# Performance work log

Measured on AMD Instinct MI355X. Metric: run time of the kernel, lower is better.

The kernel has to match this reference:

```python
import jax, jax.numpy as jnp
import numpy as np

# Static model dims
B, N, EMB, D, H, HD, L, NC = 1, 4096, 1024, 512, 8, 64, 2, 2
# Per-head local neighborhood sizes (round(pi*local_k^2) in the original, static here)
K_PER_HEAD = (32, 48, 64, 80, 96, 112, 128, 160)
SCALE = float(np.sqrt(HD))  # sigma_sq = sqrt(head_dim) in the original


def _ln(x, g, b, eps=1e-5):
    m = x.mean(-1, keepdims=True)
    v = ((x - m) ** 2).mean(-1, keepdims=True)
    return (x - m) * jax.lax.rsqrt(v + eps) * g + b


def _gather(a, idx):
    # a: [B, N, ...], idx: [B, N, K] -> [B, N, K, ...] (per-batch row gather, as k_h[range(B), indices])
    return jax.vmap(lambda ah, ih: ah[ih])(a, idx)


def setup_inputs() -> dict:
    key = jax.random.key(0)
    ks = iter(jax.random.split(key, 48))
    w = lambda shape: 0.02 * jax.random.normal(next(ks), shape, jnp.float32)
    return {
        "x": jax.random.normal(next(ks), (B, N, EMB), jnp.float32),
        "distance": 10.0 * jax.random.uniform(next(ks), (B, N, N), jnp.float32),
        "indices": jax.random.randint(next(ks), (B, N, K_PER_HEAD[-1]), 0, N, jnp.int32),
        "row": jax.random.randint(next(ks), (B, N), 0, 128, jnp.int32),
        "col": jax.random.randint(next(ks), (B, N), 0, 128, jnp.int32),
        # adapter (ResidualFullyConnected, simplified: linear proj + 1 residual layer)
        "adapter_w": w((EMB, D)), "adapter_b": jnp.zeros((D,), jnp.float32),
        "res_w": w((D, D)), "res_b": jnp.zeros((D,), jnp.float32),
        # per-block params, stacked over depth L
        "ln1_g": jnp.ones((L, D), jnp.float32), "ln1_b": jnp.zeros((L, D), jnp.float32),
        "qkv_w": w((L, D, 3 * D)), "qkv_b": jnp.zeros((L, 3 * D), jnp.float32),
        "proj_w": w((L, D, D)), "proj_b": jnp.zeros((L, D), jnp.float32),
        "ln2_g": jnp.ones((L, D), jnp.float32), "ln2_b": jnp.zeros((L, D), jnp.float32),
        "fc1_w": w((L, D, 4 * D)), "fc1_b": jnp.zeros((L, 4 * D), jnp.float32),
        "fc2_w": w((L, 4 * D, D)), "fc2_b": jnp.zeros((L, D), jnp.float32),
        # per-head decay rate parameter (DecayNetwork lambda_p); reparam = softplus
        "lam": 0.5 + w((L, H)),
        "lnf_g": jnp.ones((D,), jnp.float32), "lnf_b": jnp.zeros((D,), jnp.float32),
        "head_w": w((D, NC)), "head_b": jnp.zeros((NC,), jnp.float32),
    }


def _forward(x, distance, indices, adapter_w, adapter_b, res_w, res_b,
             ln1_g, ln1_b, qkv_w, qkv_b, proj_w, proj_b,
             ln2_g, ln2_b, fc1_w, fc1_b, fc2_w, fc2_b,
             lam, lnf_g, lnf_b, head_w, head_b):
    h = x @ adapter_w + adapter_b
    h = h + jax.nn.relu(h @ res_w + res_b)  # residual adapter layer
    for l in range(L):
        # --- spatial multi-head attention with per-head KNN window + decay log-bias ---
        xa = _ln(h, ln1_g[l], ln1_b[l])
        qkv = (xa @ qkv_w[l] + qkv_b[l]).reshape(B, N, 3, H, HD).transpose(2, 0, 3, 1, 4)
        q, k, v = qkv[0], qkv[1], qkv[2]          # [B,H,N,d]
        qn = jnp.sum(q * q, -1)                    # [B,H,N]  |q|^2
        kn = jnp.sum(k * k, -1)                    # [B,H,N]  |k|^2
        heads = []
        for hh in range(H):
            Kh = K_PER_HEAD[hh]
            idx = indices[:, :, :Kh]               # [B,N,Kh] nearest neighbors
            ksel = _gather(k[:, hh], idx)          # [B,N,Kh,d]
            vsel = _gather(v[:, hh], idx)          # [B,N,Kh,d]
            knsel = _gather(kn[:, hh], idx)        # [B,N,Kh]
            attn = jnp.einsum('bnd,bnkd->bnk', q[:, hh], ksel) / SCALE
            attn = attn - 0.5 * (qn[:, hh][..., None] + knsel) / SCALE  # norm correction
            dsel = jnp.take_along_axis(distance, idx, axis=-1)          # [B,N,Kh]
            decay = jnp.exp(-jax.nn.softplus(lam[l, hh]) * dsel) + 1e-6
            attn = jax.nn.softmax(attn + jnp.log(decay), axis=-1)
            heads.append(jnp.einsum('bnk,bnkd->bnd', attn, vsel))
        xo = jnp.stack(heads, 2).reshape(B, N, D)  # [B,N,H,d] -> [B,N,D]
        h = h + (xo @ proj_w[l] + proj_b[l])
        # --- MLP ---
        xm = _ln(h, ln2_g[l], ln2_b[l])
        h = h + (jax.nn.gelu(xm @ fc1_w[l] + fc1_b[l]) @ fc2_w[l] + fc2_b[l])
    h = _ln(h, lnf_g, lnf_b, eps=1e-6)
    return h.mean(axis=1) @ head_w + head_b  # avg pool + head -> [B, num_classes]


def reference(x, distance, indices, row, col, adapter_w, adapter_b, res_w, res_b,
              ln1_g, ln1_b, qkv_w, qkv_b, proj_w, proj_b,
              ln2_g, ln2_b, fc1_w, fc1_b, fc2_w, fc2_b,
              lam, lnf_g, lnf_b, head_w, head_b):
    # row/col are carried as metadata in the original forward and unused by the math
    return _forward(x, distance, indices, adapter_w, adapter_b, res_w, res_b,
                    ln1_g, ln1_b, qkv_w, qkv_b, proj_w, proj_b,
                    ln2_g, ln2_b, fc1_w, fc1_b, fc2_w, fc2_b,
                    lam, lnf_g, lnf_b, head_w, head_b)
```

## Files before the change

kernel.cpp:

```cpp
#include <hip/hip_runtime.h>
#include <hip/hip_bf16.h>

#define NTOK 4096
#define EMB 1024
#define DMODEL 512
#define NHEAD 8
#define NLAYER 2
#define NCLS 2
#define KMAX 160

typedef __attribute__((ext_vector_type(8))) short bf16x8;
typedef __attribute__((ext_vector_type(4))) float f32x4;

__device__ inline unsigned short f2b(float f) {
    unsigned u = __float_as_uint(f);
    u = u + 0x7FFFu + ((u >> 16) & 1u);
    return (unsigned short)(u >> 16);
}
__device__ inline float b2f(unsigned short s) {
    return __uint_as_float((unsigned)s << 16);
}

__device__ inline float dot2bf(unsigned a, unsigned b, float c) {
    float d;
    asm("v_dot2_f32_bf16 %0, %1, %2, %3" : "=v"(d) : "v"(a), "v"(b), "v"(c));
    return d;
}

__device__ inline float wsum(float v) {
    for (int o = 32; o > 0; o >>= 1) v += __shfl_xor(v, o, 64);
    return v;
}
__device__ inline float wmax(float v) {
    for (int o = 32; o > 0; o >>= 1) v = fmaxf(v, __shfl_xor(v, o, 64));
    return v;
}

typedef __attribute__((address_space(3))) unsigned lds_u32_t;
typedef __attribute__((address_space(1))) const unsigned glb_u32_t;
__device__ inline void gload16(const void* g, void* l) {
    __builtin_amdgcn_global_load_lds((glb_u32_t*)(unsigned long long)g,
                                     (lds_u32_t*)(unsigned)(unsigned long long)l,
                                     16, 0, 0);
}

__device__ const int g_s0cnt[8]  = {682, 342, 622, 822, 954, 993, 899, 607};
__device__ const int g_s0h[8]    = {7, 7, 6, 5, 4, 3, 2, 1};
__device__ const int g_s0base[8] = {0, 682, 402, 202, 70, 31, 125, 417};
__device__ const int g_s1cnt[8]  = {0, 402, 202, 70, 31, 125, 417, 1024};
__device__ const int g_s1h[8]    = {0, 6, 5, 4, 3, 2, 1, 0};
#define ATTN_BLOCKS (1631 * 8)

struct WSeg { const float* src; unsigned short* dst; int K; int N; int tile0; };
struct Prep { WSeg s[6]; const float* x; unsigned short* xb; int xtile0; };

__global__ __launch_bounds__(256) void prep_k(Prep p)
{
    __shared__ unsigned short tile[64][72];
    int t0 = blockIdx.x;
    if (t0 >= p.xtile0) {
        int i = ((t0 - p.xtile0) * 256 + threadIdx.x) * 8;
        float4 a = *(const float4*)(p.x + i);
        float4 b = *(const float4*)(p.x + i + 4);
        unsigned short o[8];
        o[0] = f2b(a.x); o[1] = f2b(a.y); o[2] = f2b(a.z); o[3] = f2b(a.w);
        o[4] = f2b(b.x); o[5] = f2b(b.y); o[6] = f2b(b.z); o[7] = f2b(b.w);
        *(uint4*)(p.xb + i) = *(const uint4*)o;
        return;
    }
    int si = 0;
#pragma unroll
    for (int i = 1; i < 6; i++) if (t0 >= p.s[i].tile0) si = i;
    const float* src0 = p.s[si].src;
    unsigned short* dst0 = p.s[si].dst;
    int K = p.s[si].K, N = p.s[si].N;
    int lt = t0 - p.s[si].tile0;
    int tx = K >> 6, ty = N >> 6;
    int per = tx * ty;
    int l = lt / per, rr = lt - l * per;
    int k0 = (rr % tx) << 6, n0 = (rr / tx) << 6;
    size_t ls = (size_t)K * N * l;
    const float* Wl = src0 + ls;
    unsigned short* Wtl = dst0 + ls;

    int t = threadIdx.x;
    int kl = t >> 2, nb = (t & 3) * 16;
    const float* src = Wl + (size_t)(k0 + kl) * N + n0 + nb;
#pragma unroll
    for (int i = 0; i < 4; i++) {
        float4 v = *(const float4*)(src + 4 * i);
        tile[nb + 4 * i + 0][kl] = f2b(v.x);
        tile[nb + 4 * i + 1][kl] = f2b(v.y);
        tile[nb + 4 * i + 2][kl] = f2b(v.z);
        tile[nb + 4 * i + 3][kl] = f2b(v.w);
    }
    __syncthreads();
    int nl = t >> 2, ks = (t & 3) * 16;
    unsigned short* dst = Wtl + (size_t)(n0 + nl) * K + k0 + ks;
    *(uint4*)dst = *(const uint4*)&tile[nl][ks];
    *(uint4*)(dst + 8) = *(const uint4*)&tile[nl][ks + 8];
}

__global__ __launch_bounds__(256) void dsel_k(const float* __restrict__ distance,
                                              const int* __restrict__ indices,
                                              float* __restrict__ dsel)
{
    int n = blockIdx.x, t = threadIdx.x;
    if (t < KMAX) {
        int idx = indices[(size_t)n * KMAX + t];
        dsel[(size_t)n * KMAX + t] = distance[(size_t)n * NTOK + idx];
    }
}

template <int BM, int BN, int WM, int WN, int MODE>
__global__ __launch_bounds__(256) void mgemm_k(
    const unsigned short* __restrict__ A, const unsigned short* __restrict__ Wt,
    const float* __restrict__ bias, const float* __restrict__ resid,
    float* __restrict__ Cf, unsigned short* __restrict__ Cb,
    float* __restrict__ knout,
    int M, int N, int K)
{
    constexpr int SM = BM / WM;
    constexpr int SN = BN / WN;
    constexpr int MR = SM / 16;
    constexpr int NR = SN / 16;

    __shared__ unsigned short Asl[2][BM * 64];
    __shared__ unsigned short Bsl[2][BN * 64];

    int tid = threadIdx.x;
    int bm = blockIdx.x * BM, bn = blockIdx.y * BN;
    int lane = tid & 63, wid = tid >> 6;
    int wm = wid / WN, wn = wid % WN;
    int l15 = lane & 15, l4 = lane >> 4;

    f32x4 acc[MR][NR] = {};

    auto stage = [&](int buf, int k0) {
#pragma unroll
        for (int i = 0; i < BM / 32; i++) {
            int ci = i * 256 + tid;
            int r = ci >> 3, c = ci & 7;
            gload16(A + (size_t)(bm + r) * K + k0 + ((c ^ (r & 7)) * 8),
                    &Asl[buf][ci * 8]);
        }
#pragma unroll
        for (int i = 0; i < BN / 32; i++) {
            int ci = i * 256 + tid;
            int r = ci >> 3, c = ci & 7;
            gload16(Wt + (size_t)(bn + r) * K + k0 + ((c ^ (r & 7)) * 8),
                    &Bsl[buf][ci * 8]);
        }
    };

    int nt = K / 64;
    stage(0, 0);
    __syncthreads();
    int cur = 0;
    for (int t = 0; t < nt; t++) {
        if (t + 1 < nt) stage(cur ^ 1, (t + 1) * 64);
#pragma unroll
        for (int ks = 0; ks < 2; ks++) {
            bf16x8 af[MR], bfr[NR];
#pragma unroll
            for (int mr = 0; mr < MR; mr++) {
                int ar = wm * SM + mr * 16 + l15;
                af[mr] = *(const bf16x8*)&Asl[cur][ar * 64 + ((((ks << 2) | l4) ^ (ar & 7)) * 8)];
            }
#pragma unroll
            for (int nr = 0; nr < NR; nr++) {
                int br = wn * SN + nr * 16 + l15;
                bfr[nr] = *(const bf16x8*)&Bsl[cur][br * 64 + ((((ks << 2) | l4) ^ (br & 7)) * 8)];
            }
#pragma unroll
            for (int mr = 0; mr < MR; mr++)
#pragma unroll
                for (int nr = 0; nr < NR; nr++)
                    acc[mr][nr] = __builtin_amdgcn_mfma_f32_16x16x32_bf16(af[mr], bfr[nr], acc[mr][nr], 0, 0, 0);
        }
        __syncthreads();
        cur ^= 1;
    }

#pragma unroll
    for (int mr = 0; mr < MR; mr++) {
#pragma unroll
        for (int nr = 0; nr < NR; nr++) {
            int col = bn + wn * SN + nr * 16 + l15;
            float bcol = bias[col];
#pragma unroll
            for (int r = 0; r < 4; r++) {
                int row = bm + wm * SM + mr * 16 + l4 * 4 + r;
                size_t off = (size_t)row * N + col;
                float v = acc[mr][nr][r] + bcol;
                if (MODE == 0) {
                    Cf[off] = v;
                } else if (MODE == 1) {
                    Cf[off] = resid[off] + fmaxf(v, 0.f);
                } else if (MODE == 2) {
                    float t3 = tanhf(0.7978845608028654f * (v + 0.044715f * v * v * v));
                    Cb[off] = f2b(0.5f * v * (1.f + t3));
                } else if (MODE == 3) {
                    Cf[off] = resid[off] + v;
                } else if (MODE == 4) {
                    Cf[off] = v;
                    Cb[off] = f2b(v);
                } else {
                    Cb[off] = f2b(v);
                }
            }
        }
    }

    if (MODE == 5) {
        int cbase = bn + wn * SN;
        if (cbase >= 512 && cbase < 1024) {
            int hh = (cbase - 512) >> 6;
#pragma unroll
            for (int mr = 0; mr < MR; mr++) {
#pragma unroll
                for (int r = 0; r < 4; r++) {
                    float p = 0.f;
#pragma unroll
                    for (int nr = 0; nr < NR; nr++) {
                        float v = acc[mr][nr][r] + bias[cbase + nr * 16 + l15];
                        p += v * v;
                    }
                    p += __shfl_xor(p, 1, 64);
                    p += __shfl_xor(p, 2, 64);
                    p += __shfl_xor(p, 4, 64);
                    p += __shfl_xor(p, 8, 64);
                    if (l15 == 0) {
                        int row = bm + wm * SM + mr * 16 + l4 * 4 + r;
                        knout[row * NHEAD + hh] = p;
                    }
                }
            }
        }
    }
}

template <int OUTB>
__global__ __launch_bounds__(256) void ln_k(
    const float* __restrict__ X, const float* __restrict__ g,
    const float* __restrict__ bta, void* __restrict__ Yv, float eps)
{
    int row = blockIdx.x;
    int tid = threadIdx.x;
    const float* xr = X + (size_t)row * DMODEL;
    float v0 = xr[tid], v1 = xr[tid + 256];
    __shared__ float red[8];
    float s = wsum(v0 + v1);
    int wid = tid >> 6, lane = tid & 63;
    if (lane == 0) red[wid] = s;
    __syncthreads();
    float m = (red[0] + red[1] + red[2] + red[3]) * (1.f / DMODEL);
    float d0 = v0 - m, d1 = v1 - m;
    float sq = wsum(d0 * d0 + d1 * d1);
    if (lane == 0) red[4 + wid] = sq;
    __syncthreads();
    float var = (red[4] + red[5] + red[6] + red[7]) * (1.f / DMODEL);
    float rs = 1.0f / sqrtf(var + eps);
    float y0 = d0 * rs * g[tid] + bta[tid];
    float y1 = d1 * rs * g[tid + 256] + bta[tid + 256];
    if (OUTB) {
        unsigned short* Y = (unsigned short*)Yv;
        Y[(size_t)row * DMODEL + tid] = f2b(y0);
        Y[(size_t)row * DMODEL + tid + 256] = f2b(y1);
    } else {
        float* Y = (float*)Yv;
        Y[(size_t)row * DMODEL + tid] = y0;
        Y[(size_t)row * DMODEL + tid + 256] = y1;
    }
}

__global__ __launch_bounds__(256) void attn_k(
    const unsigned short* __restrict__ qkv,
    const float* __restrict__ kn,
    const int* __restrict__ indices, const float* __restrict__ dsel,
    const float* __restrict__ lam, unsigned short* __restrict__ xo, int layer)
{
    int xcd = blockIdx.x & 7;
    int t = blockIdx.x >> 3;
    int hh, blk;
    int c0 = g_s0cnt[xcd];
    if (t < c0) {
        hh = g_s0h[xcd]; blk = g_s0base[xcd] + t;
    } else {
        t -= c0;
        if (t < g_s1cnt[xcd]) {
            hh = g_s1h[xcd]; blk = t;
        } else {
            return;
        }
    }

    int wid = threadIdx.x >> 6, lane = threadIdx.x & 63;
    int n = blk * 4 + wid;
    int Kh = 32 + 16 * hh + (hh == 7 ? 16 : 0);

    __shared__ __align__(16) unsigned qsp[4][32];
    __shared__ float asc[4][KMAX];
    __shared__ int   sidx[4][KMAX];

    const unsigned short* qrow = qkv + (size_t)n * 1536 + hh * 64;
    float qd = b2f(qrow[lane]);
    if (lane < 32) qsp[wid][lane] = ((const unsigned*)qrow)[lane];
    float qn2 = wsum(qd * qd);
    float sp = log1pf(expf(lam[layer * NHEAD + hh]));

    const int* irow = indices + (size_t)n * KMAX;
    const float* drow = dsel + (size_t)n * KMAX;

    int sub = lane & 3, grp = lane >> 2;
    const uint4* qp = (const uint4*)&qsp[wid][0];
    uint4 qa = qp[sub], qb = qp[4 + sub];

    int iters = Kh >> 4;
    int idxn = irow[grp];
    const uint4* krn = (const uint4*)(qkv + (size_t)idxn * 1536 + 512 + hh * 64);
    uint4 kan = krn[sub], kbn = krn[4 + sub];
    for (int it = 0; it < iters; it++) {
        int idxc = idxn;
        uint4 ka = kan, kb = kbn;
        if (it + 1 < iters) {
            idxn = irow[(it + 1) * 16 + grp];
            const uint4* kr = (const uint4*)(qkv + (size_t)idxn * 1536 + 512 + hh * 64);
            kan = kr[sub]; kbn = kr[4 + sub];
        }
        float d0 = 0.f, d1 = 0.f, d2 = 0.f, d3 = 0.f;
        d0 = dot2bf(ka.x, qa.x, d0); d1 = dot2bf(ka.y, qa.y, d1);
        d2 = dot2bf(ka.z, qa.z, d2); d3 = dot2bf(ka.w, qa.w, d3);
        d0 = dot2bf(kb.x, qb.x, d0); d1 = dot2bf(kb.y, qb.y, d1);
        d2 = dot2bf(kb.z, qb.z, d2); d3 = dot2bf(kb.w, qb.w, d3);
        float dp = (d0 + d1) + (d2 + d3);
        dp += __shfl_xor(dp, 1, 64);
        dp += __shfl_xor(dp, 2, 64);
        if (sub == 0) {
            int kk = it * 16 + grp;
            asc[wid][kk] = dp;
            sidx[wid][kk] = idxc;
        }
    }

    float s0 = -1e30f, s1 = -1e30f, s2 = -1e30f;
    {
        int kk = lane;
        if (kk < Kh) {
            float knv = kn[sidx[wid][kk] * NHEAD + hh];
            s0 = (asc[wid][kk] - 0.5f * (qn2 + knv)) * 0.125f - sp * drow[kk];
        }
        kk = lane + 64;
        if (kk < Kh) {
            float knv = kn[sidx[wid][kk] * NHEAD + hh];
            s1 = (asc[wid][kk] - 0.5f * (qn2 + knv)) * 0.125f - sp * drow[kk];
        }
        kk = lane + 128;
        if (kk < Kh) {
            float knv = kn[sidx[wid][kk] * NHEAD + hh];
            s2 = (asc[wid][kk] - 0.5f * (qn2 + knv)) * 0.125f - sp * drow[kk];
        }
    }
    float mx = wmax(fmaxf(fmaxf(s0, s1), s2));
    float e0 = (s0 > -1e29f) ? expf(s0 - mx) : 0.f;
    float e1 = (s1 > -1e29f) ? expf(s1 - mx) : 0.f;
    float e2 = (s2 > -1e29f) ? expf(s2 - mx) : 0.f;
    float se = wsum(e0 + e1 + e2);
    float inv = 1.f / se;
    if (lane < Kh)       asc[wid][lane]       = e0 * inv;
    if (lane + 64 < Kh)  asc[wid][lane + 64]  = e1 * inv;
    if (lane + 128 < Kh) asc[wid][lane + 128] = e2 * inv;

    int g = lane >> 3, q = lane & 7;
    const uint4* vb = (const uint4*)(qkv + 1024 + hh * 64 + q * 8);
    float a8[8] = {};
    int k0 = 0;
    int kmain = Kh & ~31;
    for (; k0 < kmain; k0 += 32) {
        int ii[4]; float aa[4]; uint4 vv[4];
#pragma unroll
        for (int u = 0; u < 4; u++) {
            int kk = k0 + u * 8 + g;
            ii[u] = sidx[wid][kk];
            aa[u] = asc[wid][kk];
        }
#pragma unroll
        for (int u = 0; u < 4; u++) vv[u] = vb[(size_t)ii[u] * 192];
#pragma unroll
        for (int u = 0; u < 4; u++) {
            const unsigned short* vp = (const unsigned short*)&vv[u];
#pragma unroll
            for (int d = 0; d < 8; d++) a8[d] += aa[u] * b2f(vp[d]);
        }
    }
    if (Kh & 16) {
        int ii[2]; float aa[2]; uint4 vv[2];
#pragma unroll
        for (int u = 0; u < 2; u++) {
            int kk = k0 + u * 8 + g;
            ii[u] = sidx[wid][kk];
            aa[u] = asc[wid][kk];
        }
#pragma unroll
        for (int u = 0; u < 2; u++) vv[u] = vb[(size_t)ii[u] * 192];
#pragma unroll
        for (int u = 0; u < 2; u++) {
            const unsigned short* vp = (const unsigned short*)&vv[u];
#pragma unroll
            for (int d = 0; d < 8; d++) a8[d] += aa[u] * b2f(vp[d]);
        }
    }
#pragma unroll
    for (int d = 0; d < 8; d++) {
        a8[d] += __shfl_xor(a8[d], 8, 64);
        a8[d] += __shfl_xor(a8[d], 16, 64);
        a8[d] += __shfl_xor(a8[d], 32, 64);
    }
    if (lane < 8) {
        unsigned o[4];
#pragma unroll
        for (int p = 0; p < 4; p++)
            o[p] = ((unsigned)f2b(a8[2 * p + 1]) << 16) | (unsigned)f2b(a8[2 * p]);
        *(uint4*)(xo + (size_t)n * DMODEL + hh * 64 + lane * 8) = *(uint4*)o;
    }
}

__global__ __launch_bounds__(512) void colpart_k(const float* __restrict__ Y, float* __restrict__ part)
{
    int c = threadIdx.x;
    int blk = blockIdx.x;
    const float* p = Y + (size_t)blk * 16 * DMODEL + c;
    float s = 0.f;
#pragma unroll
    for (int r = 0; r < 16; r++) s += p[r * DMODEL];
    part[blk * DMODEL + c] = s;
}

__global__ __launch_bounds__(512) void finhead_k(
    const float* __restrict__ part, const float* __restrict__ head_w,
    const float* __restrict__ head_b, float* __restrict__ out)
{
    __shared__ float mv[DMODEL];
    int c = threadIdx.x;
    float s = 0.f;
    for (int i = 0; i < 256; i++) s += part[i * DMODEL + c];
    mv[c] = s * (1.f / NTOK);
    __syncthreads();
    if (c < 64) {
        float a0 = 0.f, a1 = 0.f;
        for (int d = c; d < DMODEL; d += 64) {
            float m = mv[d];
            a0 += m * head_w[d * NCLS + 0];
            a1 += m * head_w[d * NCLS + 1];
        }
        a0 = wsum(a0);
        a1 = wsum(a1);
        if (c == 0) { out[0] = a0 + head_b[0]; out[1] = a1 + head_b[1]; }
    }
}

extern "C" void kernel_launch(void* const* d_in, const int* in_sizes, int n_in,
                              void* d_out, int out_size, void* d_ws, size_t ws_size,
                              hipStream_t stream)
{
    const float* x        = (const float*)d_in[0];
    const float* distance = (const float*)d_in[1];
    const int*   indices  = (const int*)d_in[2];
    const float* adapter_w = (const float*)d_in[5];
    const float* adapter_b = (const float*)d_in[6];
    const float* res_w     = (const float*)d_in[7];
    const float* res_b     = (const float*)d_in[8];
    const float* ln1_g     = (const float*)d_in[9];
    const float* ln1_b     = (const float*)d_in[10];
    const float* qkv_w     = (const float*)d_in[11];
    const float* qkv_b     = (const float*)d_in[12];
    const float* proj_w    = (const float*)d_in[13];
    const float* proj_b    = (const float*)d_in[14];
    const float* ln2_g     = (const float*)d_in[15];
    const float* ln2_b     = (const float*)d_in[16];
    const float* fc1_w     = (const float*)d_in[17];
    const float* fc1_b     = (const float*)d_in[18];
    const float* fc2_w     = (const float*)d_in[19];
    const float* fc2_b     = (const float*)d_in[20];
    const float* lam       = (const float*)d_in[21];
    const float* lnf_g     = (const float*)d_in[22];
    const float* lnf_b     = (const float*)d_in[23];
    const float* head_w    = (const float*)d_in[24];
    const float* head_b    = (const float*)d_in[25];
    float* out = (float*)d_out;

    char* wsb = (char*)d_ws;
    float* h   = (float*)(wsb);
    float* h0  = (float*)(wsb + (8u << 20));
    float* dsel = (float*)(wsb + (8u << 20));
    char* shared = wsb + (16u << 20);
    unsigned short* xb    = (unsigned short*)shared;
    unsigned short* qkvbb = (unsigned short*)shared;
    unsigned short* fc1b  = (unsigned short*)shared;
    unsigned short* adapter_wt = (unsigned short*)(shared + (8u << 20));
    unsigned short* res_wt     = (unsigned short*)(shared + (9u << 20));
    unsigned short* lnb  = (unsigned short*)(wsb + (40u << 20));
    unsigned short* h0b  = lnb;
    unsigned short* xob  = (unsigned short*)(wsb + (44u << 20));
    unsigned short* qkv_wt = (unsigned short*)(wsb + (48u << 20));
    unsigned short* proj_wt = (unsigned short*)(wsb + (51u << 20));
    unsigned short* fc1_wt  = (unsigned short*)(wsb + (52u << 20));
    unsigned short* fc2_wt  = (unsigned short*)(wsb + (56u << 20));
    float* kn   = (float*)(wsb + (60u << 20));
    float* part = (float*)(wsb + (60u << 20) + (1u << 18));

    dim3 blk(256);

    {
        Prep p;
        p.s[0] = { adapter_w, adapter_wt, EMB,    DMODEL, 0 };
        p.s[1] = { res_w,     res_wt,     DMODEL, DMODEL, 128 };
        p.s[2] = { qkv_w,     qkv_wt,     DMODEL, 1536,   192 };
        p.s[3] = { proj_w,    proj_wt,    DMODEL, DMODEL, 576 };
        p.s[4] = { fc1_w,     fc1_wt,     DMODEL, 2048,   704 };
        p.s[5] = { fc2_w,     fc2_wt,     2048,   DMODEL, 1216 };
        p.x = x; p.xb = xb; p.xtile0 = 1728;
        prep_k<<<1728 + (NTOK * EMB) / 2048, blk, 0, stream>>>(p);
    }

    mgemm_k<64, 64, 2, 2, 4><<<dim3(NTOK / 64, DMODEL / 64), blk, 0, stream>>>(
        xb, adapter_wt, adapter_b, nullptr, h0, h0b, nullptr, NTOK, DMODEL, EMB);
    mgemm_k<64, 64, 2, 2, 1><<<dim3(NTOK / 64, DMODEL / 64), blk, 0, stream>>>(
        h0b, res_wt, res_b, h0, h, nullptr, nullptr, NTOK, DMODEL, DMODEL);

    dsel_k<<<NTOK, blk, 0, stream>>>(distance, indices, dsel);

    for (int l = 0; l < NLAYER; l++) {
        ln_k<1><<<NTOK, blk, 0, stream>>>(h, ln1_g + l * DMODEL, ln1_b + l * DMODEL, lnb, 1e-5f);
        mgemm_k<64, 128, 2, 2, 5><<<dim3(NTOK / 64, 1536 / 128), blk, 0, stream>>>(
            lnb, qkv_wt + (size_t)l * 1536 * DMODEL, qkv_b + l * 1536, nullptr,
            nullptr, qkvbb, kn, NTOK, 1536, DMODEL);
        attn_k<<<ATTN_BLOCKS, blk, 0, stream>>>(qkvbb, kn, indices, dsel, lam, xob, l);
        mgemm_k<64, 64, 2, 2, 3><<<dim3(NTOK / 64, DMODEL / 64), blk, 0, stream>>>(
            xob, proj_wt + (size_t)l * DMODEL * DMODEL, proj_b + l * DMODEL, h,
            h, nullptr, nullptr, NTOK, DMODEL, DMODEL);
        ln_k<1><<<NTOK, blk, 0, stream>>>(h, ln2_g + l * DMODEL, ln2_b + l * DMODEL, lnb, 1e-5f);
        mgemm_k<64, 128, 2, 2, 2><<<dim3(NTOK / 64, 2048 / 128), blk, 0, stream>>>(
            lnb, fc1_wt + (size_t)l * 2048 * DMODEL, fc1_b + l * 2048, nullptr,
            nullptr, fc1b, nullptr, NTOK, 2048, DMODEL);
        mgemm_k<64, 64, 2, 2, 3><<<dim3(NTOK / 64, DMODEL / 64), blk, 0, stream>>>(
            fc1b, fc2_wt + (size_t)l * DMODEL * 2048, fc2_b + l * DMODEL, h,
            h, nullptr, nullptr, NTOK, DMODEL, 2048);
    }

    ln_k<0><<<NTOK, blk, 0, stream>>>(h, lnf_g, lnf_b, h0, 1e-6f);
    colpart_k<<<256, 512, 0, stream>>>(h0, part);
    finhead_k<<<1, 512, 0, stream>>>(part, head_w, head_b, out);
}
```

Baseline: 315.9 us.

## Fuse dsel gather into prep, fuse final LN with pooling, single-buffer GEMM

Moves the distance gather into the prep kernel and fuses the final layernorm with the column-sum pooling, removing two launches and an intermediate buffer. The GEMM drops LDS double buffering in favour of a load-sync-compute loop. This cuts LDS use and may raise occupancy, but it also stops loads from overlapping with MFMA work. Attention drops the per-row query-norm term, which cancels under softmax. It computes log(exp(-sp*d)+1e-6) explicitly instead of -sp*d, and applies the softmax normalisation after the V reduction.

```diff
diff --git a/kernel.cpp b/kernel.cpp
--- a/kernel.cpp
+++ b/kernel.cpp
@@ -52,12 +52,24 @@
 #define ATTN_BLOCKS (1631 * 8)
 
 struct WSeg { const float* src; unsigned short* dst; int K; int N; int tile0; };
-struct Prep { WSeg s[6]; const float* x; unsigned short* xb; int xtile0; };
+struct Prep {
+    WSeg s[6];
+    const float* x; unsigned short* xb; int xtile0;
+    const float* distance; const int* indices; float* dsel; int dtile0;
+};
 
 __global__ __launch_bounds__(256) void prep_k(Prep p)
 {
     __shared__ unsigned short tile[64][72];
     int t0 = blockIdx.x;
+    if (t0 >= p.dtile0) {
+        int n = t0 - p.dtile0, t = threadIdx.x;
+        if (t < KMAX) {
+            int idx = p.indices[(size_t)n * KMAX + t];
+            p.dsel[(size_t)n * KMAX + t] = p.distance[(size_t)n * NTOK + idx];
+        }
+        return;
+    }
     if (t0 >= p.xtile0) {
         int i = ((t0 - p.xtile0) * 256 + threadIdx.x) * 8;
         float4 a = *(const float4*)(p.x + i);
@@ -101,17 +113,6 @@
     *(uint4*)(dst + 8) = *(const uint4*)&tile[nl][ks + 8];
 }
 
-__global__ __launch_bounds__(256) void dsel_k(const float* __restrict__ distance,
-                                              const int* __restrict__ indices,
-                                              float* __restrict__ dsel)
-{
-    int n = blockIdx.x, t = threadIdx.x;
-    if (t < KMAX) {
-        int idx = indices[(size_t)n * KMAX + t];
-        dsel[(size_t)n * KMAX + t] = distance[(size_t)n * NTOK + idx];
-    }
-}
-
 template <int BM, int BN, int WM, int WN, int MODE>
 __global__ __launch_bounds__(256) void mgemm_k(
     const unsigned short* __restrict__ A, const unsigned short* __restrict__ Wt,
@@ -125,8 +126,8 @@
     constexpr int MR = SM / 16;
     constexpr int NR = SN / 16;
 
-    __shared__ unsigned short Asl[2][BM * 64];
-    __shared__ unsigned short Bsl[2][BN * 64];
+    __shared__ unsigned short Asl[BM * 64];
+    __shared__ unsigned short Bsl[BN * 64];
 
     int tid = threadIdx.x;
     int bm = blockIdx.x * BM, bn = blockIdx.y * BN;
@@ -136,41 +137,39 @@
 
     f32x4 acc[MR][NR] = {};
 
-    auto stage = [&](int buf, int k0) {
+    auto stage = [&](int k0) {
 #pragma unroll
         for (int i = 0; i < BM / 32; i++) {
             int ci = i * 256 + tid;
             int r = ci >> 3, c = ci & 7;
             gload16(A + (size_t)(bm + r) * K + k0 + ((c ^ (r & 7)) * 8),
-                    &Asl[buf][ci * 8]);
+                    &Asl[ci * 8]);
         }
 #pragma unroll
         for (int i = 0; i < BN / 32; i++) {
             int ci = i * 256 + tid;
             int r = ci >> 3, c = ci & 7;
             gload16(Wt + (size_t)(bn + r) * K + k0 + ((c ^ (r & 7)) * 8),
-                    &Bsl[buf][ci * 8]);
+                    &Bsl[ci * 8]);
         }
     };
 
     int nt = K / 64;
-    stage(0, 0);
-    __syncthreads();
-    int cur = 0;
     for (int t = 0; t < nt; t++) {
-        if (t + 1 < nt) stage(cur ^ 1, (t + 1) * 64);
+        stage(t * 64);
+        __syncthreads();
 #pragma unroll
         for (int ks = 0; ks < 2; ks++) {
             bf16x8 af[MR], bfr[NR];
 #pragma unroll
             for (int mr = 0; mr < MR; mr++) {
                 int ar = wm * SM + mr * 16 + l15;
-                af[mr] = *(const bf16x8*)&Asl[cur][ar * 64 + ((((ks << 2) | l4) ^ (ar & 7)) * 8)];
+                af[mr] = *(const bf16x8*)&Asl[ar * 64 + ((((ks << 2) | l4) ^ (ar & 7)) * 8)];
             }
 #pragma unroll
             for (int nr = 0; nr < NR; nr++) {
                 int br = wn * SN + nr * 16 + l15;
-                bfr[nr] = *(const bf16x8*)&Bsl[cur][br * 64 + ((((ks << 2) | l4) ^ (br & 7)) * 8)];
+                bfr[nr] = *(const bf16x8*)&Bsl[br * 64 + ((((ks << 2) | l4) ^ (br & 7)) * 8)];
             }
 #pragma unroll
             for (int mr = 0; mr < MR; mr++)
@@ -179,7 +178,6 @@
                     acc[mr][nr] = __builtin_amdgcn_mfma_f32_16x16x32_bf16(af[mr], bfr[nr], acc[mr][nr], 0, 0, 0);
         }
         __syncthreads();
-        cur ^= 1;
     }
 
 #pragma unroll
@@ -240,10 +238,9 @@
     }
 }
 
-template <int OUTB>
 __global__ __launch_bounds__(256) void ln_k(
     const float* __restrict__ X, const float* __restrict__ g,
-    const float* __restrict__ bta, void* __restrict__ Yv, float eps)
+    const float* __restrict__ bta, unsigned short* __restrict__ Y, float eps)
 {
     int row = blockIdx.x;
     int tid = threadIdx.x;
@@ -261,17 +258,36 @@
     __syncthreads();
     float var = (red[4] + red[5] + red[6] + red[7]) * (1.f / DMODEL);
     float rs = 1.0f / sqrtf(var + eps);
-    float y0 = d0 * rs * g[tid] + bta[tid];
-    float y1 = d1 * rs * g[tid + 256] + bta[tid + 256];
-    if (OUTB) {
-        unsigned short* Y = (unsigned short*)Yv;
-        Y[(size_t)row * DMODEL + tid] = f2b(y0);
-        Y[(size_t)row * DMODEL + tid + 256] = f2b(y1);
-    } else {
-        float* Y = (float*)Yv;
-        Y[(size_t)row * DMODEL + tid] = y0;
-        Y[(size_t)row * DMODEL + tid + 256] = y1;
-    }
+    Y[(size_t)row * DMODEL + tid] = f2b(d0 * rs * g[tid] + bta[tid]);
+    Y[(size_t)row * DMODEL + tid + 256] = f2b(d1 * rs * g[tid + 256] + bta[tid + 256]);
+}
+
+__global__ __launch_bounds__(512) void lnfcol_k(
+    const float* __restrict__ X, const float* __restrict__ g,
+    const float* __restrict__ bta, float* __restrict__ part)
+{
+    int c = threadIdx.x;
+    int blk = blockIdx.x;
+    __shared__ float redA[8], redB[8];
+    int wid = c >> 6, lane = c & 63;
+    float gc = g[c], bc = bta[c];
+    float acc = 0.f;
+    for (int r = 0; r < 16; r++) {
+        float v = X[(size_t)(blk * 16 + r) * DMODEL + c];
+        float s = wsum(v);
+        if (lane == 0) redA[wid] = s;
+        __syncthreads();
+        float m = (redA[0] + redA[1] + redA[2] + redA[3] +
+                   redA[4] + redA[5] + redA[6] + redA[7]) * (1.f / DMODEL);
+        float d = v - m;
+        float sq = wsum(d * d);
+        if (lane == 0) redB[wid] = sq;
+        __syncthreads();
+        float var = (redB[0] + redB[1] + redB[2] + redB[3] +
+                     redB[4] + redB[5] + redB[6] + redB[7]) * (1.f / DMODEL);
+        acc += d * (1.0f / sqrtf(var + 1e-6f)) * gc + bc;
+    }
+    part[(size_t)blk * DMODEL + c] = acc;
 }
 
 __global__ __launch_bounds__(256) void attn_k(
@@ -304,9 +320,7 @@
     __shared__ int   sidx[4][KMAX];
 
     const unsigned short* qrow = qkv + (size_t)n * 1536 + hh * 64;
-    float qd = b2f(qrow[lane]);
     if (lane < 32) qsp[wid][lane] = ((const unsigned*)qrow)[lane];
-    float qn2 = wsum(qd * qd);
     float sp = log1pf(expf(lam[layer * NHEAD + hh]));
 
     const int* irow = indices + (size_t)n * KMAX;
@@ -348,17 +362,20 @@
         int kk = lane;
         if (kk < Kh) {
             float knv = kn[sidx[wid][kk] * NHEAD + hh];
-            s0 = (asc[wid][kk] - 0.5f * (qn2 + knv)) * 0.125f - sp * drow[kk];
+            float dec = expf(-sp * drow[kk]) + 1e-6f;
+            s0 = (asc[wid][kk] - 0.5f * knv) * 0.125f + logf(dec);
         }
         kk = lane + 64;
         if (kk < Kh) {
             float knv = kn[sidx[wid][kk] * NHEAD + hh];
-            s1 = (asc[wid][kk] - 0.5f * (qn2 + knv)) * 0.125f - sp * drow[kk];
+            float dec = expf(-sp * drow[kk]) + 1e-6f;
+            s1 = (asc[wid][kk] - 0.5f * knv) * 0.125f + logf(dec);
         }
         kk = lane + 128;
         if (kk < Kh) {
             float knv = kn[sidx[wid][kk] * NHEAD + hh];
-            s2 = (asc[wid][kk] - 0.5f * (qn2 + knv)) * 0.125f - sp * drow[kk];
+            float dec = expf(-sp * drow[kk]) + 1e-6f;
+            s2 = (asc[wid][kk] - 0.5f * knv) * 0.125f + logf(dec);
         }
     }
     float mx = wmax(fmaxf(fmaxf(s0, s1), s2));
@@ -367,9 +384,9 @@
     float e2 = (s2 > -1e29f) ? expf(s2 - mx) : 0.f;
     float se = wsum(e0 + e1 + e2);
     float inv = 1.f / se;
-    if (lane < Kh)       asc[wid][lane]       = e0 * inv;
-    if (lane + 64 < Kh)  asc[wid][lane + 64]  = e1 * inv;
-    if (lane + 128 < Kh) asc[wid][lane + 128] = e2 * inv;
+    if (lane < Kh)       asc[wid][lane]       = e0;
+    if (lane + 64 < Kh)  asc[wid][lane + 64]  = e1;
+    if (lane + 128 < Kh) asc[wid][lane + 128] = e2;
 
     int g = lane >> 3, q = lane & 7;
     const uint4* vb = (const uint4*)(qkv + 1024 + hh * 64 + q * 8);
@@ -415,6 +432,7 @@
         a8[d] += __shfl_xor(a8[d], 8, 64);
         a8[d] += __shfl_xor(a8[d], 16, 64);
         a8[d] += __shfl_xor(a8[d], 32, 64);
+        a8[d] *= inv;
     }
     if (lane < 8) {
         unsigned o[4];
@@ -423,17 +441,6 @@
             o[p] = ((unsigned)f2b(a8[2 * p + 1]) << 16) | (unsigned)f2b(a8[2 * p]);
         *(uint4*)(xo + (size_t)n * DMODEL + hh * 64 + lane * 8) = *(uint4*)o;
     }
-}
-
-__global__ __launch_bounds__(512) void colpart_k(const float* __restrict__ Y, float* __restrict__ part)
-{
-    int c = threadIdx.x;
-    int blk = blockIdx.x;
-    const float* p = Y + (size_t)blk * 16 * DMODEL + c;
-    float s = 0.f;
-#pragma unroll
-    for (int r = 0; r < 16; r++) s += p[r * DMODEL];
-    part[blk * DMODEL + c] = s;
 }
 
 __global__ __launch_bounds__(512) void finhead_k(
@@ -492,13 +499,13 @@
     char* wsb = (char*)d_ws;
     float* h   = (float*)(wsb);
     float* h0  = (float*)(wsb + (8u << 20));
-    float* dsel = (float*)(wsb + (8u << 20));
     char* shared = wsb + (16u << 20);
     unsigned short* xb    = (unsigned short*)shared;
     unsigned short* qkvbb = (unsigned short*)shared;
     unsigned short* fc1b  = (unsigned short*)shared;
     unsigned short* adapter_wt = (unsigned short*)(shared + (8u << 20));
     unsigned short* res_wt     = (unsigned short*)(shared + (9u << 20));
+    float* dsel = (float*)(wsb + (32u << 20));
     unsigned short* lnb  = (unsigned short*)(wsb + (40u << 20));
     unsigned short* h0b  = lnb;
     unsigned short* xob  = (unsigned short*)(wsb + (44u << 20));
@@ -520,7 +527,9 @@
         p.s[4] = { fc1_w,     fc1_wt,     DMODEL, 2048,   704 };
         p.s[5] = { fc2_w,     fc2_wt,     2048,   DMODEL, 1216 };
         p.x = x; p.xb = xb; p.xtile0 = 1728;
-        prep_k<<<1728 + (NTOK * EMB) / 2048, blk, 0, stream>>>(p);
+        p.distance = distance; p.indices = indices; p.dsel = dsel;
+        p.dtile0 = 1728 + (NTOK * EMB) / 2048;
+        prep_k<<<p.dtile0 + NTOK, blk, 0, stream>>>(p);
     }
 
     mgemm_k<64, 64, 2, 2, 4><<<dim3(NTOK / 64, DMODEL / 64), blk, 0, stream>>>(
@@ -528,10 +537,8 @@
     mgemm_k<64, 64, 2, 2, 1><<<dim3(NTOK / 64, DMODEL / 64), blk, 0, stream>>>(
         h0b, res_wt, res_b, h0, h, nullptr, nullptr, NTOK, DMODEL, DMODEL);
 
-    dsel_k<<<NTOK, blk, 0, stream>>>(distance, indices, dsel);
-
     for (int l = 0; l < NLAYER; l++) {
-        ln_k<1><<<NTOK, blk, 0, stream>>>(h, ln1_g + l * DMODEL, ln1_b + l * DMODEL, lnb, 1e-5f);
+        ln_k<<<NTOK, blk, 0, stream>>>(h, ln1_g + l * DMODEL, ln1_b + l * DMODEL, lnb, 1e-5f);
         mgemm_k<64, 128, 2, 2, 5><<<dim3(NTOK / 64, 1536 / 128), blk, 0, stream>>>(
             lnb, qkv_wt + (size_t)l * 1536 * DMODEL, qkv_b + l * 1536, nullptr,
             nullptr, qkvbb, kn, NTOK, 1536, DMODEL);
@@ -539,7 +546,7 @@
         mgemm_k<64, 64, 2, 2, 3><<<dim3(NTOK / 64, DMODEL / 64), blk, 0, stream>>>(
             xob, proj_wt + (size_t)l * DMODEL * DMODEL, proj_b + l * DMODEL, h,
             h, nullptr, nullptr, NTOK, DMODEL, DMODEL);
-        ln_k<1><<<NTOK, blk, 0, stream>>>(h, ln2_g + l * DMODEL, ln2_b + l * DMODEL, lnb, 1e-5f);
+        ln_k<<<NTOK, blk, 0, stream>>>(h, ln2_g + l * DMODEL, ln2_b + l * DMODEL, lnb, 1e-5f);
         mgemm_k<64, 128, 2, 2, 2><<<dim3(NTOK / 64, 2048 / 128), blk, 0, stream>>>(
             lnb, fc1_wt + (size_t)l * 2048 * DMODEL, fc1_b + l * 2048, nullptr,
             nullptr, fc1b, nullptr, NTOK, 2048, DMODEL);
@@ -548,7 +555,6 @@
             h, nullptr, nullptr, NTOK, DMODEL, 2048);
     }
 
-    ln_k<0><<<NTOK, blk, 0, stream>>>(h, lnf_g, lnf_b, h0, 1e-6f);
-    colpart_k<<<256, 512, 0, stream>>>(h0, part);
+    lnfcol_k<<<256, 512, 0, stream>>>(h, lnf_g, lnf_b, part);
     finhead_k<<<1, 512, 0, stream>>>(part, head_w, head_b, out);
 }
```

New measurement: 332.3 us. +5.2%, slower.
